# Optimization experiments

Hardware: AMD Instinct MI355X
Metric: run time of the kernel (lower is better)

Reference implementation:

```python
import jax, jax.numpy as jnp
import numpy as np

K = 2            # top-k experts
TEMPERATURE = 1.0
EPS = 1e-9


def setup_inputs() -> dict:
    key = jax.random.key(0)
    k1, k2 = jax.random.split(key)
    B, S, D = 4, 4096, 4096
    G, E = 4, 64
    x = jax.random.normal(k1, (B, S, D), dtype=jnp.float32)
    # stacked gate weights, one [E, D] Linear weight per gate head
    W = jax.random.normal(k2, (G, E, D), dtype=jnp.float32) * 0.02
    return {"x": x, "W": W}


def reference(x, W):
    # per-head logits over experts: [B, S, G, E]; jitter disabled (eval / jitter_noise=0)
    logits = jnp.einsum('bsd,ged->bsge', x, W) * (1.0 / TEMPERATURE)
    probs = jax.nn.softmax(logits, axis=-1)          # softmax per head
    probs_full = probs.mean(axis=2)                  # consensus over heads: [B, S, E]
    topk_vals, idx = jax.lax.top_k(probs_full, K)    # sorted descending, matches aten.topk
    den = jnp.sum(topk_vals, axis=-1, keepdims=True)
    scores = topk_vals / jnp.maximum(den, EPS)       # clamp_min(den, 1e-9)
    pf = jax.lax.stop_gradient(probs_full)           # aux stats under no_grad
    importance = pf.mean(axis=(0, 1))                # [E]
    load = (pf > 0.0).astype(pf.dtype).mean(axis=(0, 1))  # [E]
    return idx, scores, probs_full, importance, load
```

## Files before the change

kernel.cpp:

```cpp
#include <hip/hip_runtime.h>

typedef _Float16 f16x8 __attribute__((ext_vector_type(8)));
typedef float    f32x4 __attribute__((ext_vector_type(4)));

#define MROWS 16384
#define NCOLS 256
#define KDIM  4096
#define BM    128
#define BK    32
#define LDA   40

#define OUT_SCORES 32768
#define OUT_PF     65536
#define OUT_IMP    1114112
#define OUT_LOAD   1114176

#define FIN_BLOCKS 1024

__global__ __launch_bounds__(256) void wprep(const float* __restrict__ W,
                                             _Float16* __restrict__ wfHi,
                                             _Float16* __restrict__ wfLo) {
    int t  = blockIdx.x * 256 + threadIdx.x;
    int n  = t >> 9;
    int k8 = t & 511;
    const float* src = W + ((size_t)n * KDIM + (size_t)k8 * 8);
    f16x8 hi, lo;
#pragma unroll
    for (int j = 0; j < 8; ++j) {
        float x = src[j];
        _Float16 h = (_Float16)x;
        hi[j] = h;
        lo[j] = (_Float16)(x - (float)h);
    }
    int NT  = n >> 4;
    int ksg = k8 >> 2;
    int l   = (n & 15) + ((k8 & 3) << 4);
    size_t dst = ((size_t)(ksg * 16 + NT) * 64 + (size_t)l) * 8;
    *(f16x8*)(wfHi + dst) = hi;
    *(f16x8*)(wfLo + dst) = lo;
}

__global__ __launch_bounds__(256, 2) void gemm3(const float* __restrict__ X,
        const _Float16* __restrict__ wfHi, const _Float16* __restrict__ wfLo,
        float* __restrict__ lsplit, int kQ) {
    __shared__ _Float16 aHi[2][BM * LDA];
    __shared__ _Float16 aLo[2][BM * LDA];

    const int tid  = threadIdx.x;
    const int lane = tid & 63;
    const int w    = tid >> 6;
    const int mt   = blockIdx.x & 127;
    const int s    = blockIdx.x >> 7;
    const int m0   = mt * BM;
    const int k0   = s * kQ;
    const int iters = kQ / BK;

    f32x4 acc[8][4];
#pragma unroll
    for (int a = 0; a < 8; ++a)
#pragma unroll
        for (int b = 0; b < 4; ++b) acc[a][b] = (f32x4){0.f, 0.f, 0.f, 0.f};

    const int sr = tid >> 1;
    const int sh = tid & 1;
    const float* xrow = X + ((size_t)(m0 + sr) * KDIM + (size_t)k0 + sh * 16);
    const int woff = sr * LDA + sh * 16;

    const int roff = (lane & 15) * LDA + (lane >> 4) * 8;

    size_t bbase = (((size_t)(k0 >> 5) * 16 + (size_t)w * 4) * 64 + (size_t)lane) * 8;
    const _Float16* pBH = wfHi + bbase;
    const _Float16* pBL = wfLo + bbase;

    f32x4 xq[4];
#pragma unroll
    for (int q = 0; q < 4; ++q) xq[q] = *(const f32x4*)(xrow + q * 4);

    for (int i = 0; i < iters; ++i) {
        f16x8 bH[4], bL[4];
#pragma unroll
        for (int ni = 0; ni < 4; ++ni) {
            bH[ni] = *(const f16x8*)(pBH + (size_t)ni * 512);
            bL[ni] = *(const f16x8*)(pBL + (size_t)ni * 512);
        }
        pBH += 16 * 512;
        pBL += 16 * 512;

        f32x4 xqN[4];
        {
            const float* xp = xrow + (size_t)((i + 1 < iters) ? (i + 1) : 0) * BK;
#pragma unroll
            for (int q = 0; q < 4; ++q) xqN[q] = *(const f32x4*)(xp + q * 4);
        }

        float xv[16];
#pragma unroll
        for (int q = 0; q < 4; ++q) {
            xv[q*4+0] = xq[q][0]; xv[q*4+1] = xq[q][1];
            xv[q*4+2] = xq[q][2]; xv[q*4+3] = xq[q][3];
        }
        f16x8 h0, h1, l0, l1;
#pragma unroll
        for (int j = 0; j < 8; ++j) {
            _Float16 ha = (_Float16)xv[j];
            h0[j] = ha; l0[j] = (_Float16)(xv[j] - (float)ha);
            _Float16 hb = (_Float16)xv[8 + j];
            h1[j] = hb; l1[j] = (_Float16)(xv[8 + j] - (float)hb);
        }

        _Float16* wAH = &aHi[i & 1][woff];
        _Float16* wAL = &aLo[i & 1][woff];
        *(f16x8*)(wAH)     = h0;
        *(f16x8*)(wAH + 8) = h1;
        *(f16x8*)(wAL)     = l0;
        *(f16x8*)(wAL + 8) = l1;

        asm volatile("s_waitcnt lgkmcnt(0)" ::: "memory");
        __builtin_amdgcn_s_barrier();
        __builtin_amdgcn_sched_barrier(0);

        const _Float16* rAH = &aHi[i & 1][roff];
        const _Float16* rAL = &aLo[i & 1][roff];
        __builtin_amdgcn_s_setprio(1);
#pragma unroll
        for (int mi = 0; mi < 8; ++mi) {
            f16x8 aH = *(const f16x8*)(rAH + mi * 16 * LDA);
            f16x8 aL = *(const f16x8*)(rAL + mi * 16 * LDA);
#pragma unroll
            for (int ni = 0; ni < 4; ++ni) {
                acc[mi][ni] = __builtin_amdgcn_mfma_f32_16x16x32_f16(aH, bH[ni], acc[mi][ni], 0, 0, 0);
                acc[mi][ni] = __builtin_amdgcn_mfma_f32_16x16x32_f16(aH, bL[ni], acc[mi][ni], 0, 0, 0);
                acc[mi][ni] = __builtin_amdgcn_mfma_f32_16x16x32_f16(aL, bH[ni], acc[mi][ni], 0, 0, 0);
            }
        }
        __builtin_amdgcn_s_setprio(0);

#pragma unroll
        for (int q = 0; q < 4; ++q) xq[q] = xqN[q];
    }

    float* outp = lsplit + (size_t)s * ((size_t)MROWS * NCOLS);
#pragma unroll
    for (int mi = 0; mi < 8; ++mi) {
#pragma unroll
        for (int ni = 0; ni < 4; ++ni) {
            int col   = w * 64 + ni * 16 + (lane & 15);
            int rbase = m0 + mi * 16 + ((lane >> 4) << 2);
#pragma unroll
            for (int r = 0; r < 4; ++r)
                outp[(size_t)(rbase + r) * NCOLS + col] = acc[mi][ni][r];
        }
    }
}

__global__ __launch_bounds__(256) void finalize(const float* __restrict__ lsplit,
                                                int nsplit, float* __restrict__ out,
                                                float* __restrict__ paux) {
    __shared__ float sImp[64], sLoad[64];
    const int tid = threadIdx.x;
    if (tid < 64) { sImp[tid] = 0.f; sLoad[tid] = 0.f; }
    __syncthreads();

    const int i   = tid & 15;
    const int grp = tid >> 4;
    const int r   = blockIdx.x * 16 + grp;

    float v[16];
#pragma unroll
    for (int t = 0; t < 16; ++t) {
        size_t off = (size_t)r * 256 + (size_t)i + 16 * t;
        float a = lsplit[off];
        for (int s = 1; s < nsplit; ++s)
            a += lsplit[(size_t)s * ((size_t)MROWS * NCOLS) + off];
        v[t] = a;
    }

    float hm[4];
#pragma unroll
    for (int g = 0; g < 4; ++g) {
        float m = fmaxf(fmaxf(v[4*g], v[4*g+1]), fmaxf(v[4*g+2], v[4*g+3]));
#pragma unroll
        for (int msk = 1; msk < 16; msk <<= 1)
            m = fmaxf(m, __shfl_xor(m, msk));
        hm[g] = m;
    }
    float p[16], inv[4];
#pragma unroll
    for (int g = 0; g < 4; ++g) {
        float sa = 0.f;
#pragma unroll
        for (int q = 0; q < 4; ++q) { p[4*g+q] = __expf(v[4*g+q] - hm[g]); sa += p[4*g+q]; }
#pragma unroll
        for (int msk = 1; msk < 16; msk <<= 1)
            sa += __shfl_xor(sa, msk);
        inv[g] = 1.f / sa;
    }

    float pf[4];
#pragma unroll
    for (int et = 0; et < 4; ++et) {
        pf[et] = 0.25f * (p[et] * inv[0] + p[4+et] * inv[1] + p[8+et] * inv[2] + p[12+et] * inv[3]);
        out[OUT_PF + (size_t)r * 64 + i + 16 * et] = pf[et];
        atomicAdd(&sImp[i + 16 * et], pf[et]);
        atomicAdd(&sLoad[i + 16 * et], pf[et] > 0.f ? 1.f : 0.f);
    }

    float v1 = -3.4e38f, v2 = -3.4e38f; int e1 = 0, e2 = 0;
#pragma unroll
    for (int et = 0; et < 4; ++et) {
        int e = i + 16 * et; float val = pf[et];
        if (val > v1) { v2 = v1; e2 = e1; v1 = val; e1 = e; }
        else if (val > v2) { v2 = val; e2 = e; }
    }
#pragma unroll
    for (int msk = 1; msk < 16; msk <<= 1) {
        float o1 = __shfl_xor(v1, msk); int oe1 = __shfl_xor(e1, msk);
        float o2 = __shfl_xor(v2, msk); int oe2 = __shfl_xor(e2, msk);
        bool ob = (o1 > v1) || (o1 == v1 && oe1 < e1);
        if (ob) {
            bool vb = (v1 > o2) || (v1 == o2 && e1 < oe2);
            v2 = vb ? v1 : o2; e2 = vb ? e1 : oe2;
            v1 = o1; e1 = oe1;
        } else {
            bool nb = (o1 > v2) || (o1 == v2 && oe1 < e2);
            v2 = nb ? o1 : v2; e2 = nb ? oe1 : e2;
        }
    }
    if (i == 0) {
        float den = fmaxf(v1 + v2, 1e-9f);
        out[(size_t)r * 2]              = (float)e1;
        out[(size_t)r * 2 + 1]          = (float)e2;
        out[OUT_SCORES + (size_t)r * 2]     = v1 / den;
        out[OUT_SCORES + (size_t)r * 2 + 1] = v2 / den;
    }
    __syncthreads();
    if (tid < 128)
        paux[(size_t)blockIdx.x * 128 + tid] = (tid < 64) ? sImp[tid] : sLoad[tid - 64];
}

__global__ __launch_bounds__(128) void reduce_aux(const float* __restrict__ paux,
                                                  float* __restrict__ out) {
    const int t = threadIdx.x;
    float s = 0.f;
    for (int b = 0; b < FIN_BLOCKS; ++b)
        s += paux[(size_t)b * 128 + t];
    out[OUT_IMP + t] = s * (1.0f / 16384.0f);
}

extern "C" void kernel_launch(void* const* d_in, const int* in_sizes, int n_in,
                              void* d_out, int out_size, void* d_ws, size_t ws_size,
                              hipStream_t stream) {
    const float* X = (const float*)d_in[0];
    const float* W = (const float*)d_in[1];
    float* out = (float*)d_out;
    char* ws = (char*)d_ws;

    _Float16* wfHi = (_Float16*)ws;
    _Float16* wfLo = (_Float16*)(ws + (2u << 20));
    float* lsplit  = (float*)(ws + (4u << 20));

    const size_t per = 16u << 20;
    int nsplit = (ws_size >= (4u << 20) + 4 * per + (1u << 20)) ? 4
               : (ws_size >= (4u << 20) + 2 * per + (1u << 20)) ? 2 : 1;

    float* paux = (float*)(ws + (4u << 20) + (size_t)nsplit * per);

    wprep<<<512, 256, 0, stream>>>(W, wfHi, wfLo);
    gemm3<<<128 * nsplit, 256, 0, stream>>>(X, wfHi, wfLo, lsplit, KDIM / nsplit);
    finalize<<<FIN_BLOCKS, 256, 0, stream>>>(lsplit, nsplit, out, paux);
    reduce_aux<<<1, 128, 0, stream>>>(paux, out);
}
```

Baseline: 454.0 us.

## Switch GEMM to 32x32x16 MFMA tiles and parallelize aux reduction

Moves the split-fp16 GEMM from 16x16x32 to 32x32x16 MFMA instructions. This changes the W fragment layout in wprep, the B-fragment loads, the LDS read offsets (with LDA padding changed to 34) and the epilogue row mapping. The larger MFMA tile reduces LDS/register fragment traffic per FLOP. Separately, reduce_aux now uses 1024 threads with a shared-memory partial sum instead of one 128-thread serial loop. Risks include LDS bank conflicts with the new odd-ish padding and alignment of 16-byte LDS reads (34 halves per row gives a 68-byte stride, which is not 16-byte aligned).

Measured after the change: 494.4 us. 1.09x slower.

```diff
diff --git a/kernel.cpp b/kernel.cpp
--- a/kernel.cpp
+++ b/kernel.cpp
@@ -1,14 +1,15 @@
 #include <hip/hip_runtime.h>
 
-typedef _Float16 f16x8 __attribute__((ext_vector_type(8)));
-typedef float    f32x4 __attribute__((ext_vector_type(4)));
+typedef _Float16 f16x8  __attribute__((ext_vector_type(8)));
+typedef float    f32x4  __attribute__((ext_vector_type(4)));
+typedef float    f32x16 __attribute__((ext_vector_type(16)));
 
 #define MROWS 16384
 #define NCOLS 256
 #define KDIM  4096
 #define BM    128
 #define BK    32
-#define LDA   40
+#define LDA   34
 
 #define OUT_SCORES 32768
 #define OUT_PF     65536
@@ -32,10 +33,11 @@
         hi[j] = h;
         lo[j] = (_Float16)(x - (float)h);
     }
-    int NT  = n >> 4;
-    int ksg = k8 >> 2;
-    int l   = (n & 15) + ((k8 & 3) << 4);
-    size_t dst = ((size_t)(ksg * 16 + NT) * 64 + (size_t)l) * 8;
+    int NT    = n >> 5;
+    int ksg   = k8 >> 2;
+    int ksub  = (k8 >> 1) & 1;
+    int lane  = (n & 31) + ((k8 & 1) << 5);
+    size_t dst = ((size_t)((ksg * 8 + NT) * 2 + ksub) * 64 + (size_t)lane) * 8;
     *(f16x8*)(wfHi + dst) = hi;
     *(f16x8*)(wfLo + dst) = lo;
 }
@@ -55,20 +57,22 @@
     const int k0   = s * kQ;
     const int iters = kQ / BK;
 
-    f32x4 acc[8][4];
-#pragma unroll
-    for (int a = 0; a < 8; ++a)
-#pragma unroll
-        for (int b = 0; b < 4; ++b) acc[a][b] = (f32x4){0.f, 0.f, 0.f, 0.f};
+    f32x16 acc[4][2];
+#pragma unroll
+    for (int a = 0; a < 4; ++a)
+#pragma unroll
+        for (int b = 0; b < 2; ++b)
+#pragma unroll
+            for (int q = 0; q < 16; ++q) acc[a][b][q] = 0.f;
 
     const int sr = tid >> 1;
     const int sh = tid & 1;
     const float* xrow = X + ((size_t)(m0 + sr) * KDIM + (size_t)k0 + sh * 16);
     const int woff = sr * LDA + sh * 16;
 
-    const int roff = (lane & 15) * LDA + (lane >> 4) * 8;
-
-    size_t bbase = (((size_t)(k0 >> 5) * 16 + (size_t)w * 4) * 64 + (size_t)lane) * 8;
+    const int roff = (lane & 31) * LDA + (lane >> 5) * 8;
+
+    size_t bbase = (size_t)(k0 >> 5) * 8192 + (size_t)(2 * w) * 1024 + (size_t)lane * 8;
     const _Float16* pBH = wfHi + bbase;
     const _Float16* pBL = wfLo + bbase;
 
@@ -77,14 +81,16 @@
     for (int q = 0; q < 4; ++q) xq[q] = *(const f32x4*)(xrow + q * 4);
 
     for (int i = 0; i < iters; ++i) {
-        f16x8 bH[4], bL[4];
-#pragma unroll
-        for (int ni = 0; ni < 4; ++ni) {
-            bH[ni] = *(const f16x8*)(pBH + (size_t)ni * 512);
-            bL[ni] = *(const f16x8*)(pBL + (size_t)ni * 512);
-        }
-        pBH += 16 * 512;
-        pBL += 16 * 512;
+        f16x8 bH[2][2], bL[2][2];
+#pragma unroll
+        for (int ni = 0; ni < 2; ++ni)
+#pragma unroll
+            for (int ks = 0; ks < 2; ++ks) {
+                bH[ni][ks] = *(const f16x8*)(pBH + ni * 1024 + ks * 512);
+                bL[ni][ks] = *(const f16x8*)(pBL + ni * 1024 + ks * 512);
+            }
+        pBH += 8192;
+        pBL += 8192;
 
         f32x4 xqN[4];
         {
@@ -123,14 +129,19 @@
         const _Float16* rAL = &aLo[i & 1][roff];
         __builtin_amdgcn_s_setprio(1);
 #pragma unroll
-        for (int mi = 0; mi < 8; ++mi) {
-            f16x8 aH = *(const f16x8*)(rAH + mi * 16 * LDA);
-            f16x8 aL = *(const f16x8*)(rAL + mi * 16 * LDA);
-#pragma unroll
-            for (int ni = 0; ni < 4; ++ni) {
-                acc[mi][ni] = __builtin_amdgcn_mfma_f32_16x16x32_f16(aH, bH[ni], acc[mi][ni], 0, 0, 0);
-                acc[mi][ni] = __builtin_amdgcn_mfma_f32_16x16x32_f16(aH, bL[ni], acc[mi][ni], 0, 0, 0);
-                acc[mi][ni] = __builtin_amdgcn_mfma_f32_16x16x32_f16(aL, bH[ni], acc[mi][ni], 0, 0, 0);
+        for (int mi = 0; mi < 4; ++mi) {
+            f16x8 aH0 = *(const f16x8*)(rAH + mi * 32 * LDA);
+            f16x8 aH1 = *(const f16x8*)(rAH + mi * 32 * LDA + 16);
+            f16x8 aL0 = *(const f16x8*)(rAL + mi * 32 * LDA);
+            f16x8 aL1 = *(const f16x8*)(rAL + mi * 32 * LDA + 16);
+#pragma unroll
+            for (int ni = 0; ni < 2; ++ni) {
+                acc[mi][ni] = __builtin_amdgcn_mfma_f32_32x32x16_f16(aH0, bH[ni][0], acc[mi][ni], 0, 0, 0);
+                acc[mi][ni] = __builtin_amdgcn_mfma_f32_32x32x16_f16(aH1, bH[ni][1], acc[mi][ni], 0, 0, 0);
+                acc[mi][ni] = __builtin_amdgcn_mfma_f32_32x32x16_f16(aH0, bL[ni][0], acc[mi][ni], 0, 0, 0);
+                acc[mi][ni] = __builtin_amdgcn_mfma_f32_32x32x16_f16(aH1, bL[ni][1], acc[mi][ni], 0, 0, 0);
+                acc[mi][ni] = __builtin_amdgcn_mfma_f32_32x32x16_f16(aL0, bH[ni][0], acc[mi][ni], 0, 0, 0);
+                acc[mi][ni] = __builtin_amdgcn_mfma_f32_32x32x16_f16(aL1, bH[ni][1], acc[mi][ni], 0, 0, 0);
             }
         }
         __builtin_amdgcn_s_setprio(0);
@@ -141,14 +152,16 @@
 
     float* outp = lsplit + (size_t)s * ((size_t)MROWS * NCOLS);
 #pragma unroll
-    for (int mi = 0; mi < 8; ++mi) {
-#pragma unroll
-        for (int ni = 0; ni < 4; ++ni) {
-            int col   = w * 64 + ni * 16 + (lane & 15);
-            int rbase = m0 + mi * 16 + ((lane >> 4) << 2);
-#pragma unroll
-            for (int r = 0; r < 4; ++r)
-                outp[(size_t)(rbase + r) * NCOLS + col] = acc[mi][ni][r];
+    for (int mi = 0; mi < 4; ++mi) {
+#pragma unroll
+        for (int ni = 0; ni < 2; ++ni) {
+            int col   = w * 64 + ni * 32 + (lane & 31);
+            int rbase = m0 + mi * 32 + ((lane >> 5) << 2);
+#pragma unroll
+            for (int reg = 0; reg < 16; ++reg) {
+                int row = rbase + (reg & 3) + ((reg >> 2) << 3);
+                outp[(size_t)row * NCOLS + col] = acc[mi][ni][reg];
+            }
         }
     }
 }
@@ -238,13 +251,22 @@
         paux[(size_t)blockIdx.x * 128 + tid] = (tid < 64) ? sImp[tid] : sLoad[tid - 64];
 }
 
-__global__ __launch_bounds__(128) void reduce_aux(const float* __restrict__ paux,
-                                                  float* __restrict__ out) {
-    const int t = threadIdx.x;
+__global__ __launch_bounds__(1024) void reduce_aux(const float* __restrict__ paux,
+                                                   float* __restrict__ out) {
+    __shared__ float part[8][128];
+    const int t = threadIdx.x & 127;
+    const int g = threadIdx.x >> 7;
     float s = 0.f;
-    for (int b = 0; b < FIN_BLOCKS; ++b)
+    for (int b = g * 128; b < g * 128 + 128; ++b)
         s += paux[(size_t)b * 128 + t];
-    out[OUT_IMP + t] = s * (1.0f / 16384.0f);
+    part[g][t] = s;
+    __syncthreads();
+    if (threadIdx.x < 128) {
+        float a = 0.f;
+#pragma unroll
+        for (int g2 = 0; g2 < 8; ++g2) a += part[g2][t];
+        out[OUT_IMP + t] = a * (1.0f / 16384.0f);
+    }
 }
 
 extern "C" void kernel_launch(void* const* d_in, const int* in_sizes, int n_in,
@@ -268,5 +290,5 @@
     wprep<<<512, 256, 0, stream>>>(W, wfHi, wfLo);
     gemm3<<<128 * nsplit, 256, 0, stream>>>(X, wfHi, wfLo, lsplit, KDIM / nsplit);
     finalize<<<FIN_BLOCKS, 256, 0, stream>>>(lsplit, nsplit, out, paux);
-    reduce_aux<<<1, 128, 0, stream>>>(paux, out);
-}
+    reduce_aux<<<1, 1024, 0, stream>>>(paux, out);
+}
```
